# Optimization experiments

Hardware: AMD Instinct MI355X
Metric: run time of the kernel (lower is better)

The kernel has to match this reference:

```python
import jax, jax.numpy as jnp
import numpy as np

DIM = 64
HID = DIM // 8  # 8, hidden width of pos_fc / attn_fc
B, N, V = 1024, 64, 8
NUM_IDS = 10


def setup_inputs() -> dict:
    key = jax.random.key(0)
    ks = jax.random.split(key, 24)
    stdv = 1.0 / np.sqrt(DIM * DIM)
    inp = {
        "q": jax.random.normal(ks[0], (B, N, DIM), jnp.float32),
        "k": jax.random.normal(ks[1], (B, N, V, DIM), jnp.float32),
        "pos": jax.random.normal(ks[2], (B, N, V, 4), jnp.float32),
        "strength": jax.random.normal(ks[3], (512,), jnp.float32),
        # learned params
        "q_tbl": jax.random.uniform(ks[4], (NUM_IDS, DIM * DIM), jnp.float32, -stdv, stdv),
        "k_tbl": jax.random.uniform(ks[5], (NUM_IDS, DIM * DIM), jnp.float32, -stdv, stdv),
        "v_tbl": jax.random.uniform(ks[6], (NUM_IDS, DIM * DIM), jnp.float32, -stdv, stdv),
        "pos_w1": jax.random.normal(ks[7], (4, HID), jnp.float32) * 0.5,
        "pos_b1": jax.random.normal(ks[8], (HID,), jnp.float32) * 0.1,
        "pos_w2": jax.random.normal(ks[9], (HID, DIM), jnp.float32) * 0.2,
        "pos_b2": jax.random.normal(ks[10], (DIM,), jnp.float32) * 0.1,
        "attn_w1": jax.random.normal(ks[11], (DIM, HID), jnp.float32) * 0.1,
        "attn_b1": jax.random.normal(ks[12], (HID,), jnp.float32) * 0.1,
        "attn_w2": jax.random.normal(ks[13], (HID, DIM), jnp.float32) * 0.2,
        "attn_b2": jax.random.normal(ks[14], (DIM,), jnp.float32) * 0.1,
        "out_w": jax.random.normal(ks[15], (DIM, DIM), jnp.float32) * 0.1,
        "out_b": jax.random.normal(ks[16], (DIM,), jnp.float32) * 0.1,
        "str_w": jax.random.normal(ks[17], (512, DIM), jnp.float32) * 0.04,
        "str_b": jax.random.normal(ks[18], (DIM,), jnp.float32) * 0.1,
        # int args
        "mask": jax.random.randint(ks[19], (B, N, V, 1), 0, 2, jnp.int32),
        "embed_id1": 3,
    }
    return inp


def reference(q, k, pos, strength, q_tbl, k_tbl, v_tbl,
              pos_w1, pos_b1, pos_w2, pos_b2,
              attn_w1, attn_b1, attn_w2, attn_b2,
              out_w, out_b, str_w, str_b, mask, embed_id1):
    s = strength @ str_w + str_b                       # [DIM]
    Wq = q_tbl[embed_id1].reshape(DIM, DIM)
    Wk = k_tbl[embed_id1].reshape(DIM, DIM)
    Wv = v_tbl[embed_id1].reshape(DIM, DIM)
    # F.linear(x, W) = x @ W.T ; note v is computed from k (as in source)
    qh = q @ Wq.T + s                                  # [B,N,DIM]
    kh = k @ Wk.T + s                                  # [B,N,V,DIM]
    vh = k @ Wv.T + s                                  # [B,N,V,DIM]
    p = jax.nn.relu(pos @ pos_w1 + pos_b1) @ pos_w2 + pos_b2   # [B,N,V,DIM]
    attn = kh - qh[:, :, None, :] + p                  # [B,N,V,DIM]
    attn = jax.nn.relu(attn @ attn_w1 + attn_b1) @ attn_w2 + attn_b2
    attn = jnp.where(mask == 0, jnp.float32(-1e9), attn)
    attn = jax.nn.softmax(attn, axis=-2)               # softmax over views V
    x = ((vh + p) * attn).sum(axis=2)                  # [B,N,DIM]
    x = x @ out_w + out_b
    return x
```

## Files before the change

kernel.cpp:

```cpp
#include <hip/hip_runtime.h>

#define TBL 4096

#define WS_S    0
#define WS_AT   64
#define WS_BQT  (64 + 512)
#define WS_CT   (64 + 1024)
#define WS_C0   (64 + 1024 + 64)

typedef __attribute__((ext_vector_type(8))) short bf16x8;
typedef __attribute__((ext_vector_type(4))) float f32x4;

__device__ inline short f2bf(float f) {
    union { float f; unsigned u; } v; v.f = f;
    unsigned r = v.u + 0x7fffu + ((v.u >> 16) & 1u);
    return (short)(r >> 16);
}

__device__ inline bf16x8 pack8(const float* x) {
    bf16x8 r;
    #pragma unroll
    for (int i = 0; i < 8; ++i) r[i] = f2bf(x[i]);
    return r;
}

__device__ inline bf16x8 loadpack(const float* p) {
    float4 a = *(const float4*)p;
    float4 b = *(const float4*)(p + 4);
    float t[8] = {a.x, a.y, a.z, a.w, b.x, b.y, b.z, b.w};
    return pack8(t);
}

__device__ inline bf16x8 loadpackneg(const float* p) {
    float4 a = *(const float4*)p;
    float4 b = *(const float4*)(p + 4);
    float t[8] = {-a.x, -a.y, -a.z, -a.w, -b.x, -b.y, -b.z, -b.w};
    return pack8(t);
}

__global__ __launch_bounds__(256) void precompute_kernel(
    const float* __restrict__ strength, const float* __restrict__ str_w,
    const float* __restrict__ str_b,
    const float* __restrict__ q_tbl, const float* __restrict__ k_tbl,
    const float* __restrict__ attn_w1, const float* __restrict__ attn_b1,
    const float* __restrict__ pos_w2, const float* __restrict__ pos_b2,
    const int* __restrict__ embed_id, float* __restrict__ ws)
{
    __shared__ float red[4][64];
    const int t = threadIdx.x;
    const int blk = blockIdx.x;
    const int id = embed_id[0];
    if (blk == 0) {
        const int d = t & 63, part = t >> 6;
        float acc = 0.f;
        for (int i = part * 128; i < part * 128 + 128; ++i)
            acc += strength[i] * str_w[i * 64 + d];
        red[part][d] = acc;
        __syncthreads();
        if (t < 64)
            ws[WS_S + t] = red[0][t] + red[1][t] + red[2][t] + red[3][t] + str_b[t];
    } else if (blk <= 2) {
        const int h = (blk - 1) * 4 + (t >> 6);
        const int j = t & 63;
        const float* W = k_tbl + (size_t)id * TBL;
        float acc = 0.f;
        for (int d = 0; d < 64; ++d) acc += W[d * 64 + j] * attn_w1[d * 8 + h];
        ws[WS_AT + h * 64 + j] = acc;
    } else if (blk <= 4) {
        const int h = (blk - 3) * 4 + (t >> 6);
        const int j = t & 63;
        const float* W = q_tbl + (size_t)id * TBL;
        float acc = 0.f;
        for (int d = 0; d < 64; ++d) acc += W[d * 64 + j] * attn_w1[d * 8 + h];
        ws[WS_BQT + h * 64 + j] = acc;
    } else {
        if (t < 64) {
            const int h = t >> 3, g = t & 7;
            float acc = 0.f;
            for (int d = 0; d < 64; ++d) acc += pos_w2[g * 64 + d] * attn_w1[d * 8 + h];
            ws[WS_CT + t] = acc;
        } else if (t < 72) {
            const int h = t - 64;
            float acc = attn_b1[h];
            for (int d = 0; d < 64; ++d) acc += pos_b2[d] * attn_w1[d * 8 + h];
            ws[WS_C0 + h] = acc;
        }
    }
}

__global__ __launch_bounds__(256, 3) void attn2d_main(
    const float* __restrict__ q, const float* __restrict__ k,
    const float* __restrict__ pos, const float* __restrict__ v_tbl,
    const float* __restrict__ pos_w1, const float* __restrict__ pos_b1,
    const float* __restrict__ pos_w2, const float* __restrict__ pos_b2,
    const float* __restrict__ attn_w2, const float* __restrict__ attn_b2,
    const float* __restrict__ out_w, const float* __restrict__ out_b,
    const int* __restrict__ mask, const int* __restrict__ embed_id,
    const float* __restrict__ ws, float* __restrict__ out)
{
    __shared__ float vh_lds[4][16 * 68];
    __shared__ float x_lds[4][16 * 68];
    __shared__ float rhid_lds[4][16 * 12];
    __shared__ float hp_lds[4][16 * 8];

    const int tid  = threadIdx.x;
    const int lane = tid & 63;
    const int wiv  = __builtin_amdgcn_readfirstlane(tid >> 6);
    const int q4   = lane >> 4;
    const int col  = lane & 15;

    float* vh_w = vh_lds[wiv];
    float* x_w  = x_lds[wiv];
    float* rh_w = rhid_lds[wiv];
    float* hp_w = hp_lds[wiv];

    const int wid = blockIdx.x * 4 + wiv;
    const int id  = embed_id[0];

    bf16x8 Bv[4][2];
    #pragma unroll
    for (int t = 0; t < 4; ++t)
        #pragma unroll
        for (int c = 0; c < 2; ++c)
            Bv[t][c] = loadpack(v_tbl + (size_t)id * TBL +
                                (t * 16 + col) * 64 + c * 32 + q4 * 8);
    bf16x8 Bh[4];
    {
        bf16x8 z{};
        #pragma unroll
        for (int c = 0; c < 2; ++c)
            Bh[c] = (col < 8) ? loadpack(ws + WS_AT + col * 64 + c * 32 + q4 * 8) : z;
        #pragma unroll
        for (int c = 0; c < 2; ++c)
            Bh[2 + c] = (col < 8) ? loadpackneg(ws + WS_BQT + col * 64 + c * 32 + q4 * 8) : z;
    }
    bf16x8 Bct{};
    if (q4 == 0 && col < 8) Bct = loadpack(ws + WS_CT + col * 8);

    float w2ar[8], pw2r[8];
    #pragma unroll
    for (int h = 0; h < 8; ++h) w2ar[h] = attn_w2[h * 64 + lane];
    #pragma unroll
    for (int g = 0; g < 8; ++g) pw2r[g] = pos_w2[g * 64 + lane];
    const float sr   = ws[WS_S + lane];
    const float b2pr = pos_b2[lane];
    const float b2ar = attn_b2[lane];
    const float c0r  = (col < 8) ? ws[WS_C0 + col] : 0.f;

    #pragma unroll
    for (int it = 0; it < 4; ++it) {
        const int pair = wid * 4 + it;
        const int bn0  = pair * 2;

        bf16x8 Ak[2], Aq[2];
        #pragma unroll
        for (int c = 0; c < 2; ++c)
            Ak[c] = loadpack(k + ((size_t)pair * 16 + col) * 64 + c * 32 + q4 * 8);
        #pragma unroll
        for (int c = 0; c < 2; ++c)
            Aq[c] = loadpack(q + (size_t)(bn0 + (col >> 3)) * 64 + c * 32 + q4 * 8);

        bf16x8 Ahp{};
        if (lane < 16) {
            float4 pp = *(const float4*)(pos + ((size_t)pair * 16 + lane) * 4);
            float hv[8];
            #pragma unroll
            for (int g = 0; g < 8; ++g)
                hv[g] = fmaxf(pos_b1[g] + pp.x * pos_w1[g] + pp.y * pos_w1[8 + g] +
                              pp.z * pos_w1[16 + g] + pp.w * pos_w1[24 + g], 0.f);
            *(float4*)&hp_w[lane * 8]     = make_float4(hv[0], hv[1], hv[2], hv[3]);
            *(float4*)&hp_w[lane * 8 + 4] = make_float4(hv[4], hv[5], hv[6], hv[7]);
            Ahp = pack8(hv);
        }

        f32x4 acch = {0.f, 0.f, 0.f, 0.f};
        acch = __builtin_amdgcn_mfma_f32_16x16x32_bf16(Ak[0], Bh[0], acch, 0, 0, 0);
        acch = __builtin_amdgcn_mfma_f32_16x16x32_bf16(Ak[1], Bh[1], acch, 0, 0, 0);
        acch = __builtin_amdgcn_mfma_f32_16x16x32_bf16(Aq[0], Bh[2], acch, 0, 0, 0);
        acch = __builtin_amdgcn_mfma_f32_16x16x32_bf16(Aq[1], Bh[3], acch, 0, 0, 0);
        acch = __builtin_amdgcn_mfma_f32_16x16x32_bf16(Ahp,   Bct,   acch, 0, 0, 0);
        if (col < 8) {
            #pragma unroll
            for (int r = 0; r < 4; ++r)
                rh_w[(q4 * 4 + r) * 12 + col] = fmaxf(acch[r] + c0r, 0.f);
        }

        #pragma unroll
        for (int t = 0; t < 4; ++t) {
            f32x4 a = {0.f, 0.f, 0.f, 0.f};
            a = __builtin_amdgcn_mfma_f32_16x16x32_bf16(Ak[0], Bv[t][0], a, 0, 0, 0);
            a = __builtin_amdgcn_mfma_f32_16x16x32_bf16(Ak[1], Bv[t][1], a, 0, 0, 0);
            #pragma unroll
            for (int r = 0; r < 4; ++r)
                vh_w[(q4 * 4 + r) * 68 + t * 16 + col] = a[r];
        }

        #pragma unroll
        for (int bnp = 0; bnp < 2; ++bnp) {
            const int rb = bnp * 8;
            float att[8];
            #pragma unroll
            for (int v = 0; v < 8; ++v) {
                const float* rr = &rh_w[(rb + v) * 12];
                float4 r0 = *(const float4*)rr;
                float4 r1 = *(const float4*)(rr + 4);
                float a = b2ar
                        + r0.x * w2ar[0] + r0.y * w2ar[1] + r0.z * w2ar[2] + r0.w * w2ar[3]
                        + r1.x * w2ar[4] + r1.y * w2ar[5] + r1.z * w2ar[6] + r1.w * w2ar[7];
                att[v] = (mask[(size_t)(bn0 + bnp) * 8 + v] != 0) ? a : -1e9f;
            }
            float m = att[0];
            #pragma unroll
            for (int v = 1; v < 8; ++v) m = fmaxf(m, att[v]);
            float wgt[8], ssum = 0.f;
            #pragma unroll
            for (int v = 0; v < 8; ++v) { wgt[v] = __expf(att[v] - m); ssum += wgt[v]; }
            const float inv = __builtin_amdgcn_rcpf(ssum);
            float xacc = 0.f;
            #pragma unroll
            for (int v = 0; v < 8; ++v) {
                const float* hr = &hp_w[(rb + v) * 8];
                float4 h0 = *(const float4*)hr;
                float4 h1 = *(const float4*)(hr + 4);
                float pv = sr + b2pr
                         + h0.x * pw2r[0] + h0.y * pw2r[1] + h0.z * pw2r[2] + h0.w * pw2r[3]
                         + h1.x * pw2r[4] + h1.y * pw2r[5] + h1.z * pw2r[6] + h1.w * pw2r[7];
                xacc += (wgt[v] * inv) * (vh_w[(rb + v) * 68 + lane] + pv);
            }
            x_w[(it * 2 + bnp) * 68 + lane] = xacc;
        }
    }

    bf16x8 Ax[2];
    #pragma unroll
    for (int c = 0; c < 2; ++c)
        Ax[c] = loadpack(&x_w[col * 68 + c * 32 + q4 * 8]);
    #pragma unroll
    for (int t = 0; t < 4; ++t) {
        bf16x8 Bo0, Bo1;
        {
            float t0[8], t1[8];
            #pragma unroll
            for (int jj = 0; jj < 8; ++jj) {
                t0[jj] = out_w[(q4 * 8 + jj) * 64 + t * 16 + col];
                t1[jj] = out_w[(32 + q4 * 8 + jj) * 64 + t * 16 + col];
            }
            Bo0 = pack8(t0); Bo1 = pack8(t1);
        }
        f32x4 a = {0.f, 0.f, 0.f, 0.f};
        a = __builtin_amdgcn_mfma_f32_16x16x32_bf16(Ax[0], Bo0, a, 0, 0, 0);
        a = __builtin_amdgcn_mfma_f32_16x16x32_bf16(Ax[1], Bo1, a, 0, 0, 0);
        const float ob = out_b[t * 16 + col];
        #pragma unroll
        for (int r = 0; r < 4; ++r) {
            const int row = q4 * 4 + r;
            if (row < 8)
                out[((size_t)wid * 8 + row) * 64 + t * 16 + col] = a[r] + ob;
        }
    }
}

extern "C" void kernel_launch(void* const* d_in, const int* in_sizes, int n_in,
                              void* d_out, int out_size, void* d_ws, size_t ws_size,
                              hipStream_t stream) {
    const float* q        = (const float*)d_in[0];
    const float* k        = (const float*)d_in[1];
    const float* pos      = (const float*)d_in[2];
    const float* strength = (const float*)d_in[3];
    const float* q_tbl    = (const float*)d_in[4];
    const float* k_tbl    = (const float*)d_in[5];
    const float* v_tbl    = (const float*)d_in[6];
    const float* pos_w1   = (const float*)d_in[7];
    const float* pos_b1   = (const float*)d_in[8];
    const float* pos_w2   = (const float*)d_in[9];
    const float* pos_b2   = (const float*)d_in[10];
    const float* attn_w1  = (const float*)d_in[11];
    const float* attn_b1  = (const float*)d_in[12];
    const float* attn_w2  = (const float*)d_in[13];
    const float* attn_b2  = (const float*)d_in[14];
    const float* out_w    = (const float*)d_in[15];
    const float* out_b    = (const float*)d_in[16];
    const float* str_w    = (const float*)d_in[17];
    const float* str_b    = (const float*)d_in[18];
    const int*   mask     = (const int*)d_in[19];
    const int*   embed    = (const int*)d_in[20];
    float* ws  = (float*)d_ws;
    float* out = (float*)d_out;

    hipLaunchKernelGGL(precompute_kernel, dim3(6), dim3(256), 0, stream,
                       strength, str_w, str_b, q_tbl, k_tbl, attn_w1, attn_b1,
                       pos_w2, pos_b2, embed, ws);
    hipLaunchKernelGGL(attn2d_main, dim3(2048), dim3(256), 0, stream,
                       q, k, pos, v_tbl, pos_w1, pos_b1, pos_w2, pos_b2,
                       attn_w2, attn_b2, out_w, out_b, mask, embed, ws, out);
}
```

Measured before the change: 288.8 us.

## Move attn_fc second layer and pos_fc output into MFMA, softmax in registers

Replaces the per-lane scalar FMA loops for attn_w2 and pos_w2 with extra bf16 MFMA instructions. The pos projection is accumulated directly into the value-projection accumulator. The softmax over views now runs on the MFMA output layout in registers using cross-lane shuffles, which removes the vh and hp LDS staging buffers and their round trips. In exchange it adds more bf16 rounding of the hidden activations and attention logits, and an extra LDS read of the relu hidden layer to build the A operand.

```diff
diff --git a/kernel.cpp b/kernel.cpp
--- a/kernel.cpp
+++ b/kernel.cpp
@@ -98,10 +98,8 @@
     const int* __restrict__ mask, const int* __restrict__ embed_id,
     const float* __restrict__ ws, float* __restrict__ out)
 {
-    __shared__ float vh_lds[4][16 * 68];
-    __shared__ float x_lds[4][16 * 68];
     __shared__ float rhid_lds[4][16 * 12];
-    __shared__ float hp_lds[4][16 * 8];
+    __shared__ float x_lds[4][8 * 68];
 
     const int tid  = threadIdx.x;
     const int lane = tid & 63;
@@ -109,10 +107,8 @@
     const int q4   = lane >> 4;
     const int col  = lane & 15;
 
-    float* vh_w = vh_lds[wiv];
+    float* rh_w = rhid_lds[wiv];
     float* x_w  = x_lds[wiv];
-    float* rh_w = rhid_lds[wiv];
-    float* hp_w = hp_lds[wiv];
 
     const int wid = blockIdx.x * 4 + wiv;
     const int id  = embed_id[0];
@@ -136,18 +132,32 @@
     }
     bf16x8 Bct{};
     if (q4 == 0 && col < 8) Bct = loadpack(ws + WS_CT + col * 8);
-
-    float w2ar[8], pw2r[8];
-    #pragma unroll
-    for (int h = 0; h < 8; ++h) w2ar[h] = attn_w2[h * 64 + lane];
-    #pragma unroll
-    for (int g = 0; g < 8; ++g) pw2r[g] = pos_w2[g * 64 + lane];
-    const float sr   = ws[WS_S + lane];
-    const float b2pr = pos_b2[lane];
-    const float b2ar = attn_b2[lane];
-    const float c0r  = (col < 8) ? ws[WS_C0 + col] : 0.f;
-
-    #pragma unroll
+    bf16x8 Bw2[4], Bpw2[4];
+    {
+        bf16x8 z{};
+        #pragma unroll
+        for (int t = 0; t < 4; ++t) {
+            if (q4 == 0) {
+                float t0[8], t1[8];
+                #pragma unroll
+                for (int j = 0; j < 8; ++j) {
+                    t0[j] = attn_w2[j * 64 + t * 16 + col];
+                    t1[j] = pos_w2[j * 64 + t * 16 + col];
+                }
+                Bw2[t] = pack8(t0); Bpw2[t] = pack8(t1);
+            } else { Bw2[t] = z; Bpw2[t] = z; }
+        }
+    }
+
+    float b2a4[4], sb4[4], ob4[4];
+    #pragma unroll
+    for (int t = 0; t < 4; ++t) {
+        b2a4[t] = attn_b2[t * 16 + col];
+        sb4[t]  = ws[WS_S + t * 16 + col] + pos_b2[t * 16 + col];
+        ob4[t]  = out_b[t * 16 + col];
+    }
+    const float c0r = (col < 8) ? ws[WS_C0 + col] : 0.f;
+
     for (int it = 0; it < 4; ++it) {
         const int pair = wid * 4 + it;
         const int bn0  = pair * 2;
@@ -159,6 +169,8 @@
         #pragma unroll
         for (int c = 0; c < 2; ++c)
             Aq[c] = loadpack(q + (size_t)(bn0 + (col >> 3)) * 64 + c * 32 + q4 * 8);
+
+        const int4 mk = *(const int4*)(mask + (size_t)pair * 16 + q4 * 4);
 
         bf16x8 Ahp{};
         if (lane < 16) {
@@ -168,8 +180,6 @@
             for (int g = 0; g < 8; ++g)
                 hv[g] = fmaxf(pos_b1[g] + pp.x * pos_w1[g] + pp.y * pos_w1[8 + g] +
                               pp.z * pos_w1[16 + g] + pp.w * pos_w1[24 + g], 0.f);
-            *(float4*)&hp_w[lane * 8]     = make_float4(hv[0], hv[1], hv[2], hv[3]);
-            *(float4*)&hp_w[lane * 8 + 4] = make_float4(hv[4], hv[5], hv[6], hv[7]);
             Ahp = pack8(hv);
         }
 
@@ -185,56 +195,44 @@
                 rh_w[(q4 * 4 + r) * 12 + col] = fmaxf(acch[r] + c0r, 0.f);
         }
 
+        bf16x8 Arh{};
+        if (lane < 16) Arh = loadpack(&rh_w[lane * 12]);
+
         #pragma unroll
         for (int t = 0; t < 4; ++t) {
-            f32x4 a = {0.f, 0.f, 0.f, 0.f};
-            a = __builtin_amdgcn_mfma_f32_16x16x32_bf16(Ak[0], Bv[t][0], a, 0, 0, 0);
-            a = __builtin_amdgcn_mfma_f32_16x16x32_bf16(Ak[1], Bv[t][1], a, 0, 0, 0);
-            #pragma unroll
-            for (int r = 0; r < 4; ++r)
-                vh_w[(q4 * 4 + r) * 68 + t * 16 + col] = a[r];
-        }
-
-        #pragma unroll
-        for (int bnp = 0; bnp < 2; ++bnp) {
-            const int rb = bnp * 8;
-            float att[8];
-            #pragma unroll
-            for (int v = 0; v < 8; ++v) {
-                const float* rr = &rh_w[(rb + v) * 12];
-                float4 r0 = *(const float4*)rr;
-                float4 r1 = *(const float4*)(rr + 4);
-                float a = b2ar
-                        + r0.x * w2ar[0] + r0.y * w2ar[1] + r0.z * w2ar[2] + r0.w * w2ar[3]
-                        + r1.x * w2ar[4] + r1.y * w2ar[5] + r1.z * w2ar[6] + r1.w * w2ar[7];
-                att[v] = (mask[(size_t)(bn0 + bnp) * 8 + v] != 0) ? a : -1e9f;
-            }
-            float m = att[0];
-            #pragma unroll
-            for (int v = 1; v < 8; ++v) m = fmaxf(m, att[v]);
-            float wgt[8], ssum = 0.f;
-            #pragma unroll
-            for (int v = 0; v < 8; ++v) { wgt[v] = __expf(att[v] - m); ssum += wgt[v]; }
-            const float inv = __builtin_amdgcn_rcpf(ssum);
-            float xacc = 0.f;
-            #pragma unroll
-            for (int v = 0; v < 8; ++v) {
-                const float* hr = &hp_w[(rb + v) * 8];
-                float4 h0 = *(const float4*)hr;
-                float4 h1 = *(const float4*)(hr + 4);
-                float pv = sr + b2pr
-                         + h0.x * pw2r[0] + h0.y * pw2r[1] + h0.z * pw2r[2] + h0.w * pw2r[3]
-                         + h1.x * pw2r[4] + h1.y * pw2r[5] + h1.z * pw2r[6] + h1.w * pw2r[7];
-                xacc += (wgt[v] * inv) * (vh_w[(rb + v) * 68 + lane] + pv);
-            }
-            x_w[(it * 2 + bnp) * 68 + lane] = xacc;
-        }
-    }
-
-    bf16x8 Ax[2];
-    #pragma unroll
-    for (int c = 0; c < 2; ++c)
-        Ax[c] = loadpack(&x_w[col * 68 + c * 32 + q4 * 8]);
+            f32x4 av = {0.f, 0.f, 0.f, 0.f};
+            av = __builtin_amdgcn_mfma_f32_16x16x32_bf16(Ak[0], Bv[t][0], av, 0, 0, 0);
+            av = __builtin_amdgcn_mfma_f32_16x16x32_bf16(Ak[1], Bv[t][1], av, 0, 0, 0);
+            av = __builtin_amdgcn_mfma_f32_16x16x32_bf16(Ahp,   Bpw2[t],  av, 0, 0, 0);
+            f32x4 al = {0.f, 0.f, 0.f, 0.f};
+            al = __builtin_amdgcn_mfma_f32_16x16x32_bf16(Arh, Bw2[t], al, 0, 0, 0);
+
+            float att[4];
+            att[0] = mk.x ? (al[0] + b2a4[t]) : -1e9f;
+            att[1] = mk.y ? (al[1] + b2a4[t]) : -1e9f;
+            att[2] = mk.z ? (al[2] + b2a4[t]) : -1e9f;
+            att[3] = mk.w ? (al[3] + b2a4[t]) : -1e9f;
+
+            float mp = fmaxf(fmaxf(att[0], att[1]), fmaxf(att[2], att[3]));
+            float mm = fmaxf(mp, __shfl_xor(mp, 16));
+            float e0 = __expf(att[0] - mm), e1 = __expf(att[1] - mm);
+            float e2 = __expf(att[2] - mm), e3 = __expf(att[3] - mm);
+            float sp = e0 + e1 + e2 + e3;
+            float ss = sp + __shfl_xor(sp, 16);
+            float xp = e0 * (av[0] + sb4[t]) + e1 * (av[1] + sb4[t])
+                     + e2 * (av[2] + sb4[t]) + e3 * (av[3] + sb4[t]);
+            float x = (xp + __shfl_xor(xp, 16)) * __builtin_amdgcn_rcpf(ss);
+            if ((q4 & 1) == 0)
+                x_w[(it * 2 + (q4 >> 1)) * 68 + t * 16 + col] = x;
+        }
+    }
+
+    bf16x8 Ax[2]{};
+    if (col < 8) {
+        #pragma unroll
+        for (int c = 0; c < 2; ++c)
+            Ax[c] = loadpack(&x_w[col * 68 + c * 32 + q4 * 8]);
+    }
     #pragma unroll
     for (int t = 0; t < 4; ++t) {
         bf16x8 Bo0, Bo1;
@@ -250,12 +248,11 @@
         f32x4 a = {0.f, 0.f, 0.f, 0.f};
         a = __builtin_amdgcn_mfma_f32_16x16x32_bf16(Ax[0], Bo0, a, 0, 0, 0);
         a = __builtin_amdgcn_mfma_f32_16x16x32_bf16(Ax[1], Bo1, a, 0, 0, 0);
-        const float ob = out_b[t * 16 + col];
         #pragma unroll
         for (int r = 0; r < 4; ++r) {
             const int row = q4 * 4 + r;
             if (row < 8)
-                out[((size_t)wid * 8 + row) * 64 + t * 16 + col] = a[r] + ob;
+                out[((size_t)wid * 8 + row) * 64 + t * 16 + col] = a[r] + ob4[t];
         }
     }
 }
```

New measurement: 291.0 us. Within noise of the previous version (+0.7%).
